# Optimization experiments

Hardware: AMD Instinct MI355X
Metric: run time of the kernel (lower is better)

## Reference

```python
import jax, jax.numpy as jnp
import numpy as np
import math

B, S, D, H = 4, 2048, 2048, 16
HD = D // H  # 128


def _alibi_slopes(n_heads):
    # standard ALiBi slopes: 2^(-8/n * (h+1))
    return jnp.asarray([2.0 ** (-8.0 / n_heads * (h + 1)) for h in range(n_heads)], dtype=jnp.float32)


def setup_inputs() -> dict:
    key = jax.random.key(0)
    ks = jax.random.split(key, 10)
    w = lambda k: jax.random.normal(k, (D, D), dtype=jnp.float32) * 0.02
    b = lambda k: jax.random.normal(k, (D,), dtype=jnp.float32) * 0.01
    return {
        "hidden_states": jax.random.normal(ks[0], (B, S, D), dtype=jnp.float32),
        "Wq": w(ks[1]), "bq": b(ks[2]),
        "Wk": w(ks[3]), "bk": b(ks[4]),
        "Wv": w(ks[5]), "bv": b(ks[6]),
        "Wo": w(ks[7]), "bo": b(ks[8]),
        "alibi_slopes": _alibi_slopes(H),
    }


def reference(hidden_states, Wq, bq, Wk, bk, Wv, bv, Wo, bo, alibi_slopes):
    Bn, t, _ = hidden_states.shape
    split = lambda x: x.reshape(Bn, t, H, HD).transpose(0, 2, 1, 3)  # [B,H,S,hd]
    q = split(hidden_states @ Wq.T + bq)
    k = split(hidden_states @ Wk.T + bk)
    v = split(hidden_states @ Wv.T + bv)

    scores = jnp.einsum("bhsd,bhtd->bhst", q, k)  # [B,H,S,S]
    pos = jnp.arange(t)
    # alibi bias added BEFORE the 1/sqrt(hd) scaling, as in the torch code
    rel = (pos[None, :] - pos[:, None]).astype(scores.dtype)  # j - i
    bias = alibi_slopes[:, None, None] * rel  # [H,S,S]
    scores = (scores + bias[None]) / math.sqrt(HD)
    # grok-style tanh rescaling
    scores = 30.0 * jnp.tanh(scores / 30.0)
    causal = pos[:, None] >= pos[None, :]  # [S,S]
    scores = jnp.where(causal[None, None], scores, -jnp.inf)
    probs = jax.nn.softmax(scores, axis=-1)
    ctx = jnp.einsum("bhst,bhtd->bhsd", probs, v)
    ctx = ctx.transpose(0, 2, 1, 3).reshape(Bn, t, D)
    return ctx @ Wo.T + bo
```

## Files before the change

### kernel.cpp

```cpp
#include <hip/hip_runtime.h>

typedef unsigned int u32;
typedef unsigned short u16;
typedef __bf16 bf16x8 __attribute__((ext_vector_type(8)));
typedef float f32x4 __attribute__((ext_vector_type(4)));


__device__ __forceinline__ u16 f2bf(float f) {
  u32 u = __builtin_bit_cast(u32, f);
  u32 r = u + 0x7fffu + ((u >> 16) & 1u);
  return (u16)(r >> 16);
}

__device__ __forceinline__ void gload_lds16(const void* g, void* l) {
  __builtin_amdgcn_global_load_lds(
      (__attribute__((address_space(1))) void*)(g),
      (__attribute__((address_space(3))) void*)(l), 16, 0, 0);
}


__global__ __launch_bounds__(256) void convert_kernel(
    const float* __restrict__ hs, const float* __restrict__ wq,
    const float* __restrict__ wk, const float* __restrict__ wv,
    const float* __restrict__ wo,
    u16* __restrict__ hsb, u16* __restrict__ wqb, u16* __restrict__ wkb,
    u16* __restrict__ wvb, u16* __restrict__ wob) {
  long t = (long)blockIdx.x * 256 + threadIdx.x;
  const float* src;
  u16* dst;
  long off;
  if (t < 2097152) {
    src = hs; dst = hsb; off = t << 3;
  } else {
    long u = t - 2097152;
    int wi = (int)(u >> 19);
    off = (u & 524287) << 3;
    if (wi == 0)      { src = wq; dst = wqb; }
    else if (wi == 1) { src = wk; dst = wkb; }
    else if (wi == 2) { src = wv; dst = wvb; }
    else              { src = wo; dst = wob; }
  }
  float4 a = *(const float4*)(src + off);
  float4 b = *(const float4*)(src + off + 4);
  uint4 o;
  o.x = (u32)f2bf(a.x) | ((u32)f2bf(a.y) << 16);
  o.y = (u32)f2bf(a.z) | ((u32)f2bf(a.w) << 16);
  o.z = (u32)f2bf(b.x) | ((u32)f2bf(b.y) << 16);
  o.w = (u32)f2bf(b.z) | ((u32)f2bf(b.w) << 16);
  *(uint4*)(dst + off) = o;
}


template <int OF32>
__global__ __launch_bounds__(512, 2) void gemm256_kernel(
    const u16* __restrict__ A, const u16* __restrict__ Bw,
    const float* __restrict__ bias0, const float* __restrict__ bias1,
    const float* __restrict__ bias2, void* __restrict__ o0,
    void* __restrict__ o1, void* __restrict__ o2, int m_tiles, int n_tiles) {
  __shared__ __align__(16) char L[2][2][2][16384];

  const int tid = threadIdx.x;
  const int lane = tid & 63, w = tid >> 6;
  const int lr = lane & 15, lk = lane >> 4;
  const int wm = (w >> 2) * 128, wn = (w & 3) * 64;

  const int bid = blockIdx.x;
  const int xcd = bid & 7, loc = bid >> 3;
  const int n_idx = xcd * (n_tiles >> 3) + loc / m_tiles;
  const int m_idx = loc % m_tiles;
  const int m0 = m_idx * 256, n0 = n_idx * 256;

  const char* Ab = (const char*)A;
  const char* Bb = (const char*)Bw;

  auto stage = [&](int t, int kh, int isB) {
    const char* G = isB ? Bb : Ab;
    const int r0 = isB ? n0 : m0;
    char* Ld = &L[t & 1][isB][kh][0];
    const size_t kb = (size_t)(t * 64 + kh * 32) * 2;
#pragma unroll
    for (int j = 0; j < 2; j++) {
      const int o = j * 8192 + tid * 16;
      const int row = o >> 6;
      const int c = (o & 63) ^ (((row >> 1) & 3) << 4);
      gload_lds16(G + (size_t)(r0 + row) * 4096 + kb + c, Ld + o);
    }
  };
  auto rdA = [&](bf16x8* dst, int buf, int kh, int mset) {
#pragma unroll
    for (int m = 0; m < 4; m++) {
      const int row = wm + mset * 64 + m * 16 + lr;
      const int c = (lk * 16) ^ (((row >> 1) & 3) << 4);
      dst[m] = *(const bf16x8*)(&L[buf][0][kh][0] + row * 64 + c);
    }
  };
  auto rdB = [&](bf16x8* dst, int buf, int kh) {
#pragma unroll
    for (int n = 0; n < 4; n++) {
      const int row = wn + n * 16 + lr;
      const int c = (lk * 16) ^ (((row >> 1) & 3) << 4);
      dst[n] = *(const bf16x8*)(&L[buf][1][kh][0] + row * 64 + c);
    }
  };

  f32x4 acc[2][4][4];
#pragma unroll
  for (int s = 0; s < 2; s++)
#pragma unroll
    for (int m = 0; m < 4; m++)
#pragma unroll
      for (int n = 0; n < 4; n++) acc[s][m][n] = {0.f, 0.f, 0.f, 0.f};

  auto mm = [&](f32x4 (&ac)[4][4], bf16x8* a_, bf16x8* b_) {
    __builtin_amdgcn_s_setprio(1);
#pragma unroll
    for (int m = 0; m < 4; m++)
#pragma unroll
      for (int n = 0; n < 4; n++)
        ac[m][n] = __builtin_amdgcn_mfma_f32_16x16x32_bf16(a_[m], b_[n],
                                                           ac[m][n], 0, 0, 0);
    __builtin_amdgcn_s_setprio(0);
  };

  stage(0, 0, 0); stage(0, 0, 1); stage(0, 1, 0); stage(0, 1, 1);
  stage(1, 0, 0); stage(1, 0, 1);
  asm volatile("s_waitcnt vmcnt(4)" ::: "memory");
  asm volatile("s_barrier" ::: "memory");

  bf16x8 af[4], af2[4], bf[4];
  for (int t = 0; t < 32; ++t) {
    const int buf = t & 1;
    const int t1 = (t + 1 < 32) ? t + 1 : 31;
    const int t2 = (t + 2 < 32) ? t + 2 : 31;
    stage(t1, 1, 0);
    rdA(af, buf, 0, 0); rdB(bf, buf, 0);
    asm volatile("s_barrier" ::: "memory");
    mm(acc[0], af, bf);
    asm volatile("s_barrier" ::: "memory");
    stage(t1, 1, 1);
    rdA(af2, buf, 0, 1);
    asm volatile("s_barrier" ::: "memory");
    mm(acc[1], af2, bf);
    asm volatile("s_barrier" ::: "memory");
    stage(t2, 0, 0);
    rdA(af, buf, 1, 0); rdB(bf, buf, 1);
    asm volatile("s_barrier" ::: "memory");
    mm(acc[0], af, bf);
    asm volatile("s_barrier" ::: "memory");
    stage(t2, 0, 1);
    rdA(af2, buf, 1, 1);
    asm volatile("s_barrier" ::: "memory");
    mm(acc[1], af2, bf);
    asm volatile("s_waitcnt vmcnt(4)" ::: "memory");
    asm volatile("s_barrier" ::: "memory");
  }
  asm volatile("s_waitcnt vmcnt(0)" ::: "memory");

  const float* bias;
  void* op;
  int nl0;
  if (OF32) {
    bias = bias0; op = o0; nl0 = n0;
  } else {
    const int seg = n0 >> 11;
    bias = seg == 0 ? bias0 : (seg == 1 ? bias1 : bias2);
    op = seg == 0 ? o0 : (seg == 1 ? o1 : o2);
    nl0 = n0 & 2047;
  }
#pragma unroll
  for (int n = 0; n < 4; n++) {
    const int col = nl0 + wn + n * 16 + lr;
    const float bv = bias[col];
#pragma unroll
    for (int s = 0; s < 2; s++)
#pragma unroll
      for (int m = 0; m < 4; m++) {
        const int grow = m0 + wm + s * 64 + m * 16 + lk * 4;
#pragma unroll
        for (int r = 0; r < 4; r++) {
          const float v = acc[s][m][n][r] + bv;
          if (OF32)
            ((float*)op)[(size_t)(grow + r) * 2048 + col] = v;
          else
            ((u16*)op)[(size_t)(grow + r) * 2048 + col] = f2bf(v);
        }
      }
  }
}


__global__ __launch_bounds__(512, 2) void attn_kernel(
    const u16* __restrict__ Qm, const u16* __restrict__ Km,
    const u16* __restrict__ Vm, const float* __restrict__ slopes,
    u16* __restrict__ ctx) {
  __shared__ __align__(16) char Ks[2][64 * 256];
  __shared__ __align__(16) char Vt[2][128 * 128];
  __shared__ __align__(16) char Pb[8][16 * 128];

  const int bid = blockIdx.x;
  const int sw = (bid & 7) * 64 + (bid >> 3);
  const int bh = sw >> 3, pi = sw & 7;
  const int b = bh >> 4, h = bh & 15;
  const int NTA = 2 * pi + 2;

  const int tid = threadIdx.x;
  const int lane = tid & 63, w = tid >> 6;
  const int lr = lane & 15, lk = lane >> 4;

  const char* Qb = (const char*)Qm + (size_t)b * 2048 * 4096 + h * 256;
  const char* Kb = (const char*)Km + (size_t)b * 2048 * 4096 + h * 256;
  const char* Vb = (const char*)Vm + (size_t)b * 2048 * 4096 + h * 256;
  const float slope = slopes[h];

  const int vd0 = (tid & 15) * 8;
  const int vkv2 = tid >> 4;

  uint4 vr0, vr1;

  auto kvt_of = [&](int it) { return it < NTA ? it : it - NTA; };

  auto stageK = [&](int it, int bufi) {
    const int kv0 = kvt_of(it) * 64;
#pragma unroll
    for (int j = 0; j < 2; j++) {
      const int o = j * 8192 + tid * 16;
      const int row = o >> 8, c = (o & 255) ^ ((row & 7) << 4);
      gload_lds16(Kb + (size_t)(kv0 + row) * 4096 + c, Ks[bufi] + o);
    }
  };
  auto loadV = [&](int it) {
    const int kv0 = kvt_of(it) * 64;
    vr0 = *(const uint4*)(Vb + (size_t)(kv0 + vkv2 * 2) * 4096 + vd0 * 2);
    vr1 = *(const uint4*)(Vb + (size_t)(kv0 + vkv2 * 2 + 1) * 4096 + vd0 * 2);
  };
  auto writeV = [&](int bufi) {
    const u32* p0 = (const u32*)&vr0;
    const u32* p1 = (const u32*)&vr1;
#pragma unroll
    for (int j = 0; j < 8; j++) {
      const u32 lo = (p0[j >> 1] >> ((j & 1) * 16)) & 0xffffu;
      const u32 hi = (p1[j >> 1] >> ((j & 1) * 16)) & 0xffffu;
      const int d = vd0 + j;
      const int off = d * 128 + ((vkv2 * 4) ^ (((d ^ (d >> 3)) & 7) << 4));
      *(u32*)(Vt[bufi] + off) = lo | (hi << 16);
    }
  };

  bf16x8 qf[4];
  f32x4 pv[8];
  float rs[4];
  int q0 = 0;

  stageK(0, 0);
  loadV(0);

  for (int it = 0; it < 34; ++it) {
    const int bufi = it & 1;
    const int kv0 = kvt_of(it) * 64;

    if (it == 0 || it == NTA) {
      const int st = (it == 0) ? pi : (15 - pi);
      q0 = st * 128 + w * 16;
#pragma unroll
      for (int kc = 0; kc < 4; kc++)
        qf[kc] =
            *(const bf16x8*)(Qb + (size_t)(q0 + lr) * 4096 + kc * 64 + lk * 16);
#pragma unroll
      for (int i = 0; i < 8; i++) pv[i] = {0.f, 0.f, 0.f, 0.f};
      rs[0] = rs[1] = rs[2] = rs[3] = 0.f;
    }

    writeV(bufi);
    __syncthreads();
    if (it + 1 < 34) {
      stageK(it + 1, bufi ^ 1);
      loadV(it + 1);
    }

    f32x4 sc[4];
    __builtin_amdgcn_s_setprio(1);
#pragma unroll
    for (int nb = 0; nb < 4; nb++) {
      f32x4 a = {0.f, 0.f, 0.f, 0.f};
      const int krow = nb * 16 + lr;
#pragma unroll
      for (int kc = 0; kc < 4; kc++) {
        const int off = krow * 256 + ((kc * 64 + lk * 16) ^ ((krow & 7) << 4));
        bf16x8 kf = *(const bf16x8*)(Ks[bufi] + off);
        a = __builtin_amdgcn_mfma_f32_16x16x32_bf16(qf[kc], kf, a, 0, 0, 0);
      }
      sc[nb] = a;
    }
    __builtin_amdgcn_s_setprio(0);

#pragma unroll
    for (int nb = 0; nb < 4; nb++) {
      const int kv = kv0 + nb * 16 + lr;
#pragma unroll
      for (int r = 0; r < 4; r++) {
        const int q = q0 + lk * 4 + r;
        float z = (sc[nb][r] + slope * (float)(kv - q)) * 0.08838834764831845f;
        float e2 = exp2f(z * 0.09617966939259756f);
        float p = exp2f(-86.56170245333781f * __builtin_amdgcn_rcpf(e2 + 1.0f));
        p = (kv <= q) ? p : 0.0f;
        rs[r] += p;
        const int qq = lk * 4 + r;
        const int off = qq * 128 + (((nb * 16 + lr) * 2) ^ ((qq & 7) << 4));
        *(u16*)(Pb[w] + off) = f2bf(p);
      }
    }

    __builtin_amdgcn_s_setprio(1);
#pragma unroll
    for (int kc = 0; kc < 2; kc++) {
      const int poff = lr * 128 + ((kc * 64 + lk * 16) ^ ((lr & 7) << 4));
      bf16x8 pf = *(const bf16x8*)(Pb[w] + poff);
#pragma unroll
      for (int db = 0; db < 8; db++) {
        const int d = db * 16 + lr;
        const int voff =
            d * 128 + ((kc * 64 + lk * 16) ^ (((d ^ (d >> 3)) & 7) << 4));
        bf16x8 vf = *(const bf16x8*)(Vt[bufi] + voff);
        pv[db] = __builtin_amdgcn_mfma_f32_16x16x32_bf16(pf, vf, pv[db], 0, 0, 0);
      }
    }
    __builtin_amdgcn_s_setprio(0);

    if (it == NTA - 1 || it == 33) {
      float inv[4];
#pragma unroll
      for (int r = 0; r < 4; r++) {
        float s = rs[r];
        s += __shfl_xor(s, 1);
        s += __shfl_xor(s, 2);
        s += __shfl_xor(s, 4);
        s += __shfl_xor(s, 8);
        inv[r] = 1.0f / s;
      }
      const size_t baserow = (size_t)b * 2048 + q0 + lk * 4;
#pragma unroll
      for (int db = 0; db < 8; db++)
#pragma unroll
        for (int r = 0; r < 4; r++)
          ctx[(baserow + r) * 2048 + h * 128 + db * 16 + lr] =
              f2bf(pv[db][r] * inv[r]);
    }
  }
}


extern "C" void kernel_launch(void* const* d_in, const int* in_sizes, int n_in,
                              void* d_out, int out_size, void* d_ws,
                              size_t ws_size, hipStream_t stream) {
  const float* hs = (const float*)d_in[0];
  const float* Wq = (const float*)d_in[1];
  const float* bq = (const float*)d_in[2];
  const float* Wk = (const float*)d_in[3];
  const float* bk = (const float*)d_in[4];
  const float* Wv = (const float*)d_in[5];
  const float* bv = (const float*)d_in[6];
  const float* Wo = (const float*)d_in[7];
  const float* bo = (const float*)d_in[8];
  const float* slopes = (const float*)d_in[9];

  char* ws = (char*)d_ws;
  u16* hsb = (u16*)(ws);
  u16* wqb = (u16*)(ws + 33554432);
  u16* wkb = (u16*)(ws + 41943040);
  u16* wvb = (u16*)(ws + 50331648);
  u16* wob = (u16*)(ws + 58720256);
  u16* Qb  = (u16*)(ws + 67108864);
  u16* Kb  = (u16*)(ws + 100663296);
  u16* Vb  = (u16*)(ws + 134217728);
  u16* ctxb = hsb;

  convert_kernel<<<16384, 256, 0, stream>>>(hs, Wq, Wk, Wv, Wo, hsb, wqb, wkb,
                                            wvb, wob);
  gemm256_kernel<0><<<768, 512, 0, stream>>>(hsb, wqb, bq, bk, bv, Qb, Kb, Vb,
                                             32, 24);
  attn_kernel<<<512, 512, 0, stream>>>(Qb, Kb, Vb, slopes, ctxb);
  gemm256_kernel<1><<<256, 512, 0, stream>>>(ctxb, wob, bo, bo, bo, d_out,
                                             d_out, d_out, 32, 8);
}
```

Baseline: 532.8 us.

## Replace tanh softcap with rational approximation and single-buffer K in LDS

Computes the softcapped score exponent using a Padé-style rational polynomial for tanh instead of two exp2 calls plus a reciprocal. Precomputes the ALiBi bias terms per lane, and uses cheaper bf16 rounding and a byte-permute V transpose. K staging drops from double to single buffer, which adds an extra barrier and a full vmcnt wait each iteration. This cuts LDS use at the cost of less overlap, and the approximation may lose accuracy for large scores.

```diff
diff --git a/kernel.cpp b/kernel.cpp
--- a/kernel.cpp
+++ b/kernel.cpp
@@ -193,7 +193,7 @@
     const u16* __restrict__ Qm, const u16* __restrict__ Km,
     const u16* __restrict__ Vm, const float* __restrict__ slopes,
     u16* __restrict__ ctx) {
-  __shared__ __align__(16) char Ks[2][64 * 256];
+  __shared__ __align__(16) char Ks[64 * 256];
   __shared__ __align__(16) char Vt[2][128 * 128];
   __shared__ __align__(16) char Pb[8][16 * 128];
 
@@ -210,7 +210,20 @@
   const char* Qb = (const char*)Qm + (size_t)b * 2048 * 4096 + h * 256;
   const char* Kb = (const char*)Km + (size_t)b * 2048 * 4096 + h * 256;
   const char* Vb = (const char*)Vm + (size_t)b * 2048 * 4096 + h * 256;
-  const float slope = slopes[h];
+
+  const float SCALE = 0.08838834764831845f;
+  const float sl_c = slopes[h] * SCALE;
+
+  const float A0 = 1363.3468136400704f, A2 = 0.16831442143704573f,
+              A4 = 1.7811049887518067e-6f;
+  const float D0 = 945.0f, D2 = 0.4666666666666667f, D4 = 1.851851851851852e-5f;
+  const float SH = -43.2808512266689f;
+
+  float Tt[16];
+#pragma unroll
+  for (int nb = 0; nb < 4; nb++)
+#pragma unroll
+    for (int r = 0; r < 4; r++) Tt[nb * 4 + r] = sl_c * (float)(nb * 16 - r);
 
   const int vd0 = (tid & 15) * 8;
   const int vkv2 = tid >> 4;
@@ -219,13 +232,13 @@
 
   auto kvt_of = [&](int it) { return it < NTA ? it : it - NTA; };
 
-  auto stageK = [&](int it, int bufi) {
+  auto stageK = [&](int it) {
     const int kv0 = kvt_of(it) * 64;
 #pragma unroll
     for (int j = 0; j < 2; j++) {
       const int o = j * 8192 + tid * 16;
       const int row = o >> 8, c = (o & 255) ^ ((row & 7) << 4);
-      gload_lds16(Kb + (size_t)(kv0 + row) * 4096 + c, Ks[bufi] + o);
+      gload_lds16(Kb + (size_t)(kv0 + row) * 4096 + c, Ks + o);
     }
   };
   auto loadV = [&](int it) {
@@ -237,12 +250,14 @@
     const u32* p0 = (const u32*)&vr0;
     const u32* p1 = (const u32*)&vr1;
 #pragma unroll
-    for (int j = 0; j < 8; j++) {
-      const u32 lo = (p0[j >> 1] >> ((j & 1) * 16)) & 0xffffu;
-      const u32 hi = (p1[j >> 1] >> ((j & 1) * 16)) & 0xffffu;
-      const int d = vd0 + j;
-      const int off = d * 128 + ((vkv2 * 4) ^ (((d ^ (d >> 3)) & 7) << 4));
-      *(u32*)(Vt[bufi] + off) = lo | (hi << 16);
+    for (int wd = 0; wd < 4; wd++) {
+      const u32 ev = __builtin_amdgcn_perm(p1[wd], p0[wd], 0x05040100u);
+      const u32 od = __builtin_amdgcn_perm(p1[wd], p0[wd], 0x07060302u);
+      const int d0_ = vd0 + 2 * wd, d1_ = d0_ + 1;
+      *(u32*)(Vt[bufi] + d0_ * 128 +
+              ((vkv2 * 4) ^ (((d0_ ^ (d0_ >> 3)) & 7) << 4))) = ev;
+      *(u32*)(Vt[bufi] + d1_ * 128 +
+              ((vkv2 * 4) ^ (((d1_ ^ (d1_ >> 3)) & 7) << 4))) = od;
     }
   };
 
@@ -251,7 +266,7 @@
   float rs[4];
   int q0 = 0;
 
-  stageK(0, 0);
+  stageK(0);
   loadV(0);
 
   for (int it = 0; it < 34; ++it) {
@@ -271,11 +286,10 @@
     }
 
     writeV(bufi);
+    asm volatile("s_waitcnt vmcnt(0)" ::: "memory");
     __syncthreads();
-    if (it + 1 < 34) {
-      stageK(it + 1, bufi ^ 1);
-      loadV(it + 1);
-    }
+
+    if (it + 1 < 34) loadV(it + 1);
 
     f32x4 sc[4];
     __builtin_amdgcn_s_setprio(1);
@@ -286,34 +300,43 @@
 #pragma unroll
       for (int kc = 0; kc < 4; kc++) {
         const int off = krow * 256 + ((kc * 64 + lk * 16) ^ ((krow & 7) << 4));
-        bf16x8 kf = *(const bf16x8*)(Ks[bufi] + off);
+        bf16x8 kf = *(const bf16x8*)(Ks + off);
         a = __builtin_amdgcn_mfma_f32_16x16x32_bf16(qf[kc], kf, a, 0, 0, 0);
       }
       sc[nb] = a;
     }
     __builtin_amdgcn_s_setprio(0);
 
+    __syncthreads();
+    if (it + 1 < 34) stageK(it + 1);
+
+    const float aliB = sl_c * (float)(kv0 + lr - q0 - lk * 4);
 #pragma unroll
     for (int nb = 0; nb < 4; nb++) {
       const int kv = kv0 + nb * 16 + lr;
 #pragma unroll
       for (int r = 0; r < 4; r++) {
         const int q = q0 + lk * 4 + r;
-        float z = (sc[nb][r] + slope * (float)(kv - q)) * 0.08838834764831845f;
-        float e2 = exp2f(z * 0.09617966939259756f);
-        float p = exp2f(-86.56170245333781f * __builtin_amdgcn_rcpf(e2 + 1.0f));
+        const float z = fmaf(sc[nb][r], SCALE, aliB + Tt[nb * 4 + r]);
+        const float u = z * z;
+        const float num = fmaf(u, fmaf(u, A4, A2), A0);
+        const float den = fmaf(u, fmaf(u, D4, D2), D0);
+        const float pa = fmaf(z * num, __builtin_amdgcn_rcpf(den), SH);
+        float p = exp2f(pa);
         p = (kv <= q) ? p : 0.0f;
         rs[r] += p;
         const int qq = lk * 4 + r;
-        const int off = qq * 128 + (((nb * 16 + lr) * 2) ^ ((qq & 7) << 4));
-        *(u16*)(Pb[w] + off) = f2bf(p);
+        const int off =
+            qq * 128 + (((nb * 16 + lr) * 2) ^ ((qq & 12) << 3));
+        const u32 ub = __builtin_bit_cast(u32, p);
+        *(u16*)(Pb[w] + off) = (u16)((ub + 0x8000u) >> 16);
       }
     }
 
     __builtin_amdgcn_s_setprio(1);
 #pragma unroll
     for (int kc = 0; kc < 2; kc++) {
-      const int poff = lr * 128 + ((kc * 64 + lk * 16) ^ ((lr & 7) << 4));
+      const int poff = lr * 128 + ((kc * 64 + lk * 16) ^ ((lr & 12) << 3));
       bf16x8 pf = *(const bf16x8*)(Pb[w] + poff);
 #pragma unroll
       for (int db = 0; db < 8; db++) {
```

Measured after the change: 504.0 us. 1.06x faster.
